# Kernel tuning notes

Hardware: AMD Instinct MI355X
Metric: run time of the kernel (lower is better)

Reference implementation:

```python
import jax, jax.numpy as jnp
import numpy as np

B, IN_DIM, L = 8, 1, 512
D_MODEL, N_LAYERS, D_STATE, HORIZON, D_CONV, EXPAND = 512, 4, 16, 96, 4, 2
D_INNER = EXPAND * D_MODEL            # 1024
DT_RANK = (D_MODEL + 15) // 16        # ceil(d_model/16) = 32
EPS = 1e-5


def setup_inputs() -> dict:
    key = jax.random.key(0)
    ks = jax.random.split(key, 10)
    s = 0.02
    f32 = jnp.float32
    return {
        "x": jax.random.normal(ks[0], (B, IN_DIM, L), f32),
        "embed_w": jax.random.normal(ks[1], (D_MODEL, IN_DIM), f32) * s,
        "embed_b": jnp.zeros((D_MODEL,), f32),
        "norm_w": jnp.ones((N_LAYERS, D_MODEL), f32),
        "in_proj_w": jax.random.normal(ks[2], (N_LAYERS, 2 * D_INNER, D_MODEL), f32) * s,
        "conv_w": jax.random.normal(ks[3], (N_LAYERS, D_INNER, D_CONV), f32) * s,
        "conv_b": jnp.zeros((N_LAYERS, D_INNER), f32),
        "x_proj_w": jax.random.normal(ks[4], (N_LAYERS, DT_RANK + 2 * D_STATE, D_INNER), f32) * s,
        "dt_w": jax.random.normal(ks[5], (N_LAYERS, D_INNER, DT_RANK), f32) * s,
        "dt_b": jax.random.uniform(ks[6], (N_LAYERS, D_INNER), f32, -4.0, -2.0),
        "A_log": jnp.log(jnp.broadcast_to(jnp.arange(1, D_STATE + 1, dtype=f32), (N_LAYERS, D_INNER, D_STATE))),
        "D": jnp.ones((N_LAYERS, D_INNER), f32),
        "out_proj_w": jax.random.normal(ks[7], (N_LAYERS, D_MODEL, D_INNER), f32) * s,
        "head_w": jax.random.normal(ks[8], (HORIZON, D_MODEL), f32) * s,
        "head_b": jnp.zeros((HORIZON,), f32),
    }


def _rmsnorm(x, w):
    return x * jax.lax.rsqrt(jnp.mean(x * x, axis=-1, keepdims=True) + EPS) * w


def _mamba_layer(x, norm_w, in_w, conv_w, conv_b, xproj_w, dt_w, dt_b, A_log, Dp, out_w):
    res = x
    h = _rmsnorm(x, norm_w)
    xz = h @ in_w.T                       # (B, L, 2*I)
    xin, z = jnp.split(xz, 2, axis=-1)
    # causal depthwise conv1d over L (left-pad d_conv-1)
    lhs = jnp.swapaxes(xin, 1, 2)         # (B, I, L)
    rhs = conv_w[:, None, :]              # (I, 1, K)
    conv = jax.lax.conv_general_dilated(
        lhs, rhs, (1,), [(D_CONV - 1, 0)],
        dimension_numbers=("NCH", "OIH", "NCH"), feature_group_count=D_INNER)
    xin = jax.nn.silu(jnp.swapaxes(conv, 1, 2) + conv_b)   # (B, L, I)
    dbc = xin @ xproj_w.T                                   # (B, L, dt_rank+2N)
    delta = jax.nn.softplus(dbc[..., :DT_RANK] @ dt_w.T + dt_b)  # (B, L, I)
    Bc = dbc[..., DT_RANK:DT_RANK + D_STATE]                # (B, L, N)
    Cc = dbc[..., DT_RANK + D_STATE:]                       # (B, L, N)
    A = -jnp.exp(A_log)                                     # (I, N)
    dA = jnp.exp(delta[..., None] * A)                      # (B, L, I, N)
    dBx = delta[..., None] * Bc[:, :, None, :] * xin[..., None]

    def step(hst, inputs):
        a, bx = inputs
        hst = a * hst + bx
        return hst, hst

    h0 = jnp.zeros((x.shape[0], D_INNER, D_STATE), x.dtype)
    _, hs = jax.lax.scan(step, h0, (jnp.swapaxes(dA, 0, 1), jnp.swapaxes(dBx, 0, 1)))
    hs = jnp.swapaxes(hs, 0, 1)                             # (B, L, I, N)
    y = jnp.einsum("blin,bln->bli", hs, Cc) + Dp * xin
    y = y * jax.nn.silu(z)
    return res + y @ out_w.T


def reference(x, embed_w, embed_b, norm_w, in_proj_w, conv_w, conv_b, x_proj_w,
              dt_w, dt_b, A_log, D, out_proj_w, head_w, head_b):
    h = jnp.swapaxes(x, 1, 2) @ embed_w.T + embed_b         # (B, L, d_model)
    for i in range(N_LAYERS):
        h = _mamba_layer(h, norm_w[i], in_proj_w[i], conv_w[i], conv_b[i],
                         x_proj_w[i], dt_w[i], dt_b[i], A_log[i], D[i], out_proj_w[i])
    return h[:, -1, :] @ head_w.T + head_b                  # (B, horizon)
```

## Files before the change

### kernel.cpp

```cpp
#include <hip/hip_runtime.h>
#include <hip/hip_bf16.h>

#define B_  8
#define L_  512
#define DM  512
#define NL  4
#define DS  16
#define HOR 96
#define DC  4
#define DI  1024
#define DTR 32

#define CHUNK 16
#define NCHK (L_/CHUNK)

typedef __bf16 bf16_t;
typedef __bf16 b8_t __attribute__((ext_vector_type(8)));
typedef float  f4_t __attribute__((ext_vector_type(4)));

#define LOG2E 1.44269504088896f

__device__ __forceinline__ float sigmoidf_(float x){ return 1.f/(1.f+__expf(-x)); }

__device__ __forceinline__ void async16(const bf16_t* g, bf16_t* l){
  __builtin_amdgcn_global_load_lds((const __attribute__((address_space(1))) void*)g,
                                   (__attribute__((address_space(3))) void*)l, 16, 0, 0);
}

__global__ __launch_bounds__(256) void k_cvtall(const float* __restrict__ p0, bf16_t* __restrict__ o0,
                                                const float* __restrict__ p1, bf16_t* __restrict__ o1,
                                                const float* __restrict__ p2, bf16_t* __restrict__ o2,
                                                const float* __restrict__ p3, bf16_t* __restrict__ o3){
  int j = blockIdx.x*256 + threadIdx.x;
  const int S0=1048576, S1=65536, S2=32768;
  const float* src; bf16_t* dst;
  if (j < S0){ src=p0; dst=o0; }
  else if ((j-=S0) < S1){ src=p1; dst=o1; }
  else if ((j-=S1) < S2){ src=p2; dst=o2; }
  else { j-=S2; src=p3; dst=o3; }
  f4_t v = ((const f4_t*)src)[j];
  bf16_t* o = dst + (size_t)j*4;
  o[0]=(bf16_t)v[0]; o[1]=(bf16_t)v[1]; o[2]=(bf16_t)v[2]; o[3]=(bf16_t)v[3];
}

__global__ __launch_bounds__(256) void k_embed(const float* __restrict__ x, const float* __restrict__ ew,
                                               const float* __restrict__ eb, float* __restrict__ h){
  int idx = blockIdx.x*256 + threadIdx.x;
  int d = idx & (DM-1); int t = idx >> 9;
  h[idx] = x[t]*ew[d] + eb[d];
}

__global__ __launch_bounds__(256) void k_rms(const float* __restrict__ h, const float* __restrict__ w,
                                             bf16_t* __restrict__ o){
  int t = blockIdx.x; int tid = threadIdx.x;
  const float* hp = h + (size_t)t*DM;
  float v0 = hp[tid], v1 = hp[tid+256];
  float s = v0*v0 + v1*v1;
  #pragma unroll
  for (int m=32;m;m>>=1) s += __shfl_xor(s, m);
  __shared__ float red[4];
  if ((tid&63)==0) red[tid>>6]=s;
  __syncthreads();
  float tot = red[0]+red[1]+red[2]+red[3];
  float sc = rsqrtf(tot*(1.f/DM) + 1e-5f);
  o[(size_t)t*DM + tid]       = (bf16_t)(v0*sc*w[tid]);
  o[(size_t)t*DM + tid + 256] = (bf16_t)(v1*sc*w[tid+256]);
}

__global__ __launch_bounds__(256) void k_g128(const bf16_t* __restrict__ A, int lda,
                                              const bf16_t* __restrict__ W, int ldw,
                                              int K, bf16_t* __restrict__ Cbf, int ldc){
  __shared__ bf16_t As[4*128*32];
  __shared__ bf16_t Ws[4*128*32];
  int tid = threadIdx.x;
  int m0 = blockIdx.y*128, n0 = blockIdx.x*128;
  int wave = tid>>6, lane = tid&63;
  int wm = (wave>>1)*64, wn = (wave&1)*64;
  int lr = lane&15, q = lane>>4;
  int rs = tid>>2, cs = (tid&3)*8;
  f4_t acc[4][4] = {};
  for (int k0=0;k0<K;k0+=128){
    #pragma unroll
    for (int p=0;p<4;p++){
      #pragma unroll
      for (int s=0;s<2;s++){
        int row = s*64 + rs;
        async16(A + (size_t)(m0+row)*lda + k0 + p*32 + cs, As + p*4096 + s*2048 + tid*8);
        async16(W + (size_t)(n0+row)*ldw + k0 + p*32 + cs, Ws + p*4096 + s*2048 + tid*8);
      }
    }
    __syncthreads();
    #pragma unroll
    for (int p=0;p<4;p++){
      b8_t a[4], b[4];
      #pragma unroll
      for (int i=0;i<4;i++) a[i] = *(const b8_t*)(As + p*4096 + (wm+i*16+lr)*32 + q*8);
      #pragma unroll
      for (int j=0;j<4;j++) b[j] = *(const b8_t*)(Ws + p*4096 + (wn+j*16+lr)*32 + q*8);
      #pragma unroll
      for (int i=0;i<4;i++)
        #pragma unroll
        for (int j=0;j<4;j++)
          acc[i][j] = __builtin_amdgcn_mfma_f32_16x16x32_bf16(a[i], b[j], acc[i][j], 0,0,0);
    }
    __syncthreads();
  }
  #pragma unroll
  for (int i=0;i<4;i++)
  #pragma unroll
  for (int j=0;j<4;j++){
    int col = n0 + wn + j*16 + lr;
    int rb  = m0 + wm + i*16 + q*4;
    #pragma unroll
    for (int r=0;r<4;r++)
      Cbf[(size_t)(rb+r)*ldc + col] = (bf16_t)acc[i][j][r];
  }
}

__global__ __launch_bounds__(256) void k_gout64(const bf16_t* __restrict__ A,
                                                const bf16_t* __restrict__ W,
                                                float* __restrict__ C){
  __shared__ bf16_t As[4*64*32];
  __shared__ bf16_t Ws[4*64*32];
  int tid = threadIdx.x;
  int m0 = blockIdx.y*64, n0 = blockIdx.x*64;
  int wave = tid>>6, lane = tid&63;
  int wm = (wave>>1)*32, wn = (wave&1)*32;
  int lr = lane&15, q = lane>>4;
  int e0 = tid*8, r0 = e0>>5, c0 = e0&31;
  f4_t acc[2][2] = {};
  for (int k0=0;k0<DI;k0+=128){
    #pragma unroll
    for (int p=0;p<4;p++){
      async16(A + (size_t)(m0+r0)*DI + k0 + p*32 + c0, As + p*2048 + e0);
      async16(W + (size_t)(n0+r0)*DI + k0 + p*32 + c0, Ws + p*2048 + e0);
    }
    __syncthreads();
    #pragma unroll
    for (int p=0;p<4;p++){
      b8_t a[2], b[2];
      #pragma unroll
      for (int i=0;i<2;i++) a[i] = *(const b8_t*)(As + p*2048 + (wm+i*16+lr)*32 + q*8);
      #pragma unroll
      for (int j=0;j<2;j++) b[j] = *(const b8_t*)(Ws + p*2048 + (wn+j*16+lr)*32 + q*8);
      #pragma unroll
      for (int i=0;i<2;i++)
        #pragma unroll
        for (int j=0;j<2;j++)
          acc[i][j] = __builtin_amdgcn_mfma_f32_16x16x32_bf16(a[i], b[j], acc[i][j], 0,0,0);
    }
    __syncthreads();
  }
  #pragma unroll
  for (int i=0;i<2;i++)
  #pragma unroll
  for (int j=0;j<2;j++){
    int col = n0 + wn + j*16 + lr;
    int rb  = m0 + wm + i*16 + q*4;
    #pragma unroll
    for (int r=0;r<4;r++){
      size_t off = (size_t)(rb+r)*DM + col;
      C[off] = C[off] + acc[i][j][r];
    }
  }
}

__global__ __launch_bounds__(256) void k_dbc(const bf16_t* __restrict__ xzbf, const float* __restrict__ cw,
                                             const float* __restrict__ cb, const bf16_t* __restrict__ wxp,
                                             float* __restrict__ part, bf16_t* __restrict__ xinbf){
  __shared__ bf16_t As[4*64*32];
  __shared__ bf16_t Ws[4*64*32];
  int tid = threadIdx.x;
  int m0 = blockIdx.x*64;
  int z = blockIdx.y;
  int kbase = z*256;
  int wave = tid>>6, lane = tid&63;
  int wm = (wave>>1)*32, wn = (wave&1)*32;
  int lr = lane&15, q = lane>>4;
  int e0 = tid*8, r0 = e0>>5, c0 = e0&31;
  int gt = m0 + r0;
  int l  = gt & (L_-1);
  f4_t acc[2][2] = {};
  for (int k0=0;k0<256;k0+=128){
    #pragma unroll
    for (int p=0;p<4;p++){
      int ch = kbase + k0 + p*32 + c0;
      float cv[8];
      #pragma unroll
      for (int c=0;c<8;c++) cv[c] = cb[ch+c];
      #pragma unroll
      for (int k=0;k<DC;k++){
        if (l + k - (DC-1) >= 0){
          b8_t xv = *(const b8_t*)(xzbf + (size_t)(gt + k - (DC-1))*(2*DI) + ch);
          #pragma unroll
          for (int c=0;c<8;c++) cv[c] += (float)xv[c] * cw[(ch+c)*DC + k];
        }
      }
      b8_t av;
      #pragma unroll
      for (int c=0;c<8;c++){ float s = cv[c]*sigmoidf_(cv[c]); av[c] = (bf16_t)s; }
      *(b8_t*)(As + p*2048 + e0) = av;
      *(b8_t*)(xinbf + (size_t)gt*DI + ch) = av;
      async16(wxp + (size_t)r0*DI + kbase + k0 + p*32 + c0, Ws + p*2048 + e0);
    }
    __syncthreads();
    #pragma unroll
    for (int p=0;p<4;p++){
      b8_t a[2], b[2];
      #pragma unroll
      for (int i=0;i<2;i++) a[i] = *(const b8_t*)(As + p*2048 + (wm+i*16+lr)*32 + q*8);
      #pragma unroll
      for (int j=0;j<2;j++) b[j] = *(const b8_t*)(Ws + p*2048 + (wn+j*16+lr)*32 + q*8);
      #pragma unroll
      for (int i=0;i<2;i++)
        #pragma unroll
        for (int j=0;j<2;j++)
          acc[i][j] = __builtin_amdgcn_mfma_f32_16x16x32_bf16(a[i], b[j], acc[i][j], 0,0,0);
    }
    __syncthreads();
  }
  float* P = part + (size_t)z*(B_*L_*64);
  #pragma unroll
  for (int i=0;i<2;i++)
  #pragma unroll
  for (int j=0;j<2;j++){
    int col = wn + j*16 + lr;
    int rb  = m0 + wm + i*16 + q*4;
    #pragma unroll
    for (int r=0;r<4;r++) P[(size_t)(rb+r)*64 + col] = acc[i][j][r];
  }
}

__global__ __launch_bounds__(256) void k_dt(const float* __restrict__ part, const bf16_t* __restrict__ wdt,
                                            const float* __restrict__ dtb, float* __restrict__ dbc,
                                            bf16_t* __restrict__ delta){
  __shared__ bf16_t As[64*32];
  __shared__ bf16_t Ws[64*32];
  int tid = threadIdx.x;
  int m0 = blockIdx.y*64, n0 = blockIdx.x*64;
  const size_t S = (size_t)B_*L_*64;
  int r0 = tid>>2, c0 = (tid&3)*8;
  int gt = m0 + r0;
  size_t base = (size_t)gt*64 + c0;
  f4_t s0 = *(const f4_t*)(part + base);
  f4_t s1 = *(const f4_t*)(part + base + 4);
  #pragma unroll
  for (int z=1;z<4;z++){
    s0 += *(const f4_t*)(part + z*S + base);
    s1 += *(const f4_t*)(part + z*S + base + 4);
  }
  b8_t av;
  #pragma unroll
  for (int c=0;c<4;c++){ av[c] = (bf16_t)s0[c]; av[4+c] = (bf16_t)s1[c]; }
  *(b8_t*)(As + tid*8) = av;
  if (n0 == 0){
    f4_t t0 = *(const f4_t*)(part + base + 32);
    f4_t t1 = *(const f4_t*)(part + base + 36);
    #pragma unroll
    for (int z=1;z<4;z++){
      t0 += *(const f4_t*)(part + z*S + base + 32);
      t1 += *(const f4_t*)(part + z*S + base + 36);
    }
    *(f4_t*)(dbc + base + 32) = t0;
    *(f4_t*)(dbc + base + 36) = t1;
  }
  async16(wdt + (size_t)(n0+r0)*DTR + c0, Ws + tid*8);
  __syncthreads();
  int wave = tid>>6, lane = tid&63;
  int wm = (wave>>1)*32, wn = (wave&1)*32;
  int lr = lane&15, q = lane>>4;
  b8_t a[2], b[2];
  #pragma unroll
  for (int i=0;i<2;i++) a[i] = *(const b8_t*)(As + (wm+i*16+lr)*32 + q*8);
  #pragma unroll
  for (int j=0;j<2;j++) b[j] = *(const b8_t*)(Ws + (wn+j*16+lr)*32 + q*8);
  f4_t acc[2][2] = {};
  #pragma unroll
  for (int i=0;i<2;i++)
    #pragma unroll
    for (int j=0;j<2;j++)
      acc[i][j] = __builtin_amdgcn_mfma_f32_16x16x32_bf16(a[i], b[j], acc[i][j], 0,0,0);
  #pragma unroll
  for (int i=0;i<2;i++)
  #pragma unroll
  for (int j=0;j<2;j++){
    int col = n0 + wn + j*16 + lr;
    int rb  = m0 + wm + i*16 + q*4;
    #pragma unroll
    for (int r=0;r<4;r++){
      float xv = acc[i][j][r] + dtb[col];
      float v = (xv>20.f)?xv:log1pf(__expf(xv));
      delta[(size_t)(rb+r)*DI + col] = (bf16_t)v;
    }
  }
}

__global__ __launch_bounds__(256) void k_scan_p1(const bf16_t* __restrict__ delta, const bf16_t* __restrict__ xin,
                                                 const float* __restrict__ dbc, const float* __restrict__ Alog,
                                                 bf16_t* __restrict__ hend, bf16_t* __restrict__ aprod){
  __shared__ bf16_t des[CHUNK][256];
  __shared__ bf16_t xs[CHUNK][256];
  __shared__ float Bs[CHUNK][DS];
  int tid = threadIdx.x;
  int blk = blockIdx.x;
  int chgrp = blk & 3;
  int chunk = (blk>>2) & (NCHK-1);
  int b = blk >> 7;
  int ch0 = chgrp<<8;
  int ch = ch0 + tid;
  int t0 = (b<<9) + chunk*CHUNK;
  #pragma unroll
  for (int idx=tid; idx<CHUNK*32; idx+=256){
    int row = idx>>5, c = (idx&31)*8;
    *(b8_t*)(&des[row][c]) = *(const b8_t*)(delta + (size_t)(t0+row)*DI + ch0 + c);
    *(b8_t*)(&xs[row][c])  = *(const b8_t*)(xin   + (size_t)(t0+row)*DI + ch0 + c);
  }
  {
    int ll = tid>>4, n = tid&15;
    Bs[ll][n] = dbc[(t0+ll)*64 + DTR + n];
  }
  __syncthreads();
  float An2[DS], h[DS];
  const f4_t* Ap = (const f4_t*)(Alog + ch*DS);
  #pragma unroll
  for (int v=0;v<4;v++){
    f4_t a4 = Ap[v];
    #pragma unroll
    for (int k=0;k<4;k++){ An2[v*4+k] = -__expf(a4[k])*LOG2E; h[v*4+k]=0.f; }
  }
  float sde = 0.f;
  #pragma unroll
  for (int l=0;l<CHUNK;l++){
    float de = (float)des[l][tid];
    float xv = (float)xs[l][tid];
    float dx = de*xv;
    sde += de;
    #pragma unroll
    for (int n=0;n<DS;n++){
      float dA = exp2f(de*An2[n]);
      h[n] = dA*h[n] + dx*Bs[l][n];
    }
  }
  size_t base = ((size_t)chunk*(B_*DI) + (b<<10) + ch)*DS;
  b8_t hv[2], av[2];
  #pragma unroll
  for (int v=0;v<2;v++)
    #pragma unroll
    for (int k=0;k<8;k++){
      hv[v][k] = (bf16_t)h[v*8+k];
      av[v][k] = (bf16_t)exp2f(An2[v*8+k]*sde);
    }
  ((b8_t*)(hend + base))[0] = hv[0]; ((b8_t*)(hend + base))[1] = hv[1];
  ((b8_t*)(aprod + base))[0] = av[0]; ((b8_t*)(aprod + base))[1] = av[1];
}

__global__ __launch_bounds__(256) void k_scan_p2(const bf16_t* __restrict__ hend, bf16_t* __restrict__ ap_hin){
  int g = blockIdx.x*256 + threadIdx.x;
  float h = 0.f;
  for (int c=0;c<NCHK;c++){
    size_t off = (size_t)c*(B_*DI*DS) + g;
    float a = (float)ap_hin[off];
    float e = (float)hend[off];
    ap_hin[off] = (bf16_t)h;
    h = a*h + e;
  }
}

__global__ __launch_bounds__(256) void k_scan_p3(const bf16_t* __restrict__ delta, const bf16_t* __restrict__ xz,
                                                 const bf16_t* __restrict__ xin,
                                                 const float* __restrict__ dbc, const float* __restrict__ Alog,
                                                 const bf16_t* __restrict__ hin, const float* __restrict__ Dp,
                                                 bf16_t* __restrict__ ybf){
  __shared__ bf16_t des[CHUNK][256];
  __shared__ bf16_t xs[CHUNK][256];
  __shared__ bf16_t zs[CHUNK][256];
  __shared__ float Bs[CHUNK][DS];
  __shared__ float Cs[CHUNK][DS];
  int tid = threadIdx.x;
  int blk = blockIdx.x;
  int chgrp = blk & 3;
  int chunk = (blk>>2) & (NCHK-1);
  int b = blk >> 7;
  int ch0 = chgrp<<8;
  int ch = ch0 + tid;
  int t0 = (b<<9) + chunk*CHUNK;
  #pragma unroll
  for (int idx=tid; idx<CHUNK*32; idx+=256){
    int row = idx>>5, c = (idx&31)*8;
    *(b8_t*)(&des[row][c]) = *(const b8_t*)(delta + (size_t)(t0+row)*DI + ch0 + c);
    *(b8_t*)(&xs[row][c])  = *(const b8_t*)(xin   + (size_t)(t0+row)*DI + ch0 + c);
    *(b8_t*)(&zs[row][c])  = *(const b8_t*)(xz + (size_t)(t0+row)*(2*DI) + DI + ch0 + c);
  }
  {
    int ll = tid>>4, n = tid&15;
    Bs[ll][n] = dbc[(t0+ll)*64 + DTR + n];
    Cs[ll][n] = dbc[(t0+ll)*64 + DTR + DS + n];
  }
  __syncthreads();
  float An2[DS], h[DS];
  const f4_t* Ap = (const f4_t*)(Alog + ch*DS);
  size_t base = ((size_t)chunk*(B_*DI) + (b<<10) + ch)*DS;
  b8_t h0 = ((const b8_t*)(hin + base))[0];
  b8_t h1 = ((const b8_t*)(hin + base))[1];
  #pragma unroll
  for (int v=0;v<4;v++){
    f4_t a4 = Ap[v];
    #pragma unroll
    for (int k=0;k<4;k++){
      An2[v*4+k] = -__expf(a4[k])*LOG2E;
      int idx = v*4+k;
      h[idx] = (idx<8) ? (float)h0[idx] : (float)h1[idx-8];
    }
  }
  float Dv = Dp[ch];
  bf16_t* yp = ybf + (size_t)t0*DI + ch;
  #pragma unroll
  for (int l=0;l<CHUNK;l++){
    float de = (float)des[l][tid];
    float zv = (float)zs[l][tid];
    float xv = (float)xs[l][tid];
    float dx = de*xv;
    float y = 0.f;
    #pragma unroll
    for (int n=0;n<DS;n++){
      float dA = exp2f(de*An2[n]);
      h[n] = dA*h[n] + dx*Bs[l][n];
      y += h[n]*Cs[l][n];
    }
    y = (y + Dv*xv) * (zv * sigmoidf_(zv));
    yp[(size_t)l*DI] = (bf16_t)y;
  }
}

__global__ __launch_bounds__(256) void k_head(const float* __restrict__ h, const float* __restrict__ hw,
                                              const float* __restrict__ hb, float* __restrict__ out){
  int wave = threadIdx.x>>6, lane = threadIdx.x&63;
  int gw = blockIdx.x*4 + wave;
  int b = gw / HOR, hh = gw % HOR;
  const float* hp = h + ((size_t)b*L_ + (L_-1))*DM;
  const float* wp = hw + (size_t)hh*DM;
  float s = 0.f;
  #pragma unroll
  for (int k=0;k<DM;k+=64) s += hp[k+lane]*wp[k+lane];
  #pragma unroll
  for (int m=32;m;m>>=1) s += __shfl_xor(s, m);
  if (lane==0) out[gw] = s + hb[hh];
}

extern "C" void kernel_launch(void* const* d_in, const int* in_sizes, int n_in,
                              void* d_out, int out_size, void* d_ws, size_t ws_size,
                              hipStream_t stream){
  const float* x    = (const float*)d_in[0];
  const float* ew   = (const float*)d_in[1];
  const float* eb   = (const float*)d_in[2];
  const float* nw   = (const float*)d_in[3];
  const float* ipw  = (const float*)d_in[4];
  const float* cw   = (const float*)d_in[5];
  const float* cb   = (const float*)d_in[6];
  const float* xpw  = (const float*)d_in[7];
  const float* dtw  = (const float*)d_in[8];
  const float* dtb  = (const float*)d_in[9];
  const float* alog = (const float*)d_in[10];
  const float* Dp   = (const float*)d_in[11];
  const float* opw  = (const float*)d_in[12];
  const float* hw   = (const float*)d_in[13];
  const float* hb   = (const float*)d_in[14];
  float* out = (float*)d_out;

  char* ws = (char*)d_ws;
  size_t o = 0;
  float*  h      = (float*)(ws + o);  o += (size_t)8<<20;
  bf16_t* hnorm  = (bf16_t*)(ws + o); o += (size_t)4<<20;
  bf16_t* xzbf   = (bf16_t*)(ws + o); o += (size_t)16<<20;
  bf16_t* xinbf  = (bf16_t*)(ws + o); o += (size_t)8<<20;
  bf16_t* delta  = (bf16_t*)(ws + o); o += (size_t)8<<20;
  bf16_t* ybf    = (bf16_t*)(ws + o); o += (size_t)8<<20;
  float*  dbc    = (float*)(ws + o);  o += (size_t)1<<20;
  float*  dbcp   = (float*)(ws + o);  o += (size_t)4<<20;
  bf16_t* w_in   = (bf16_t*)(ws + o); o += (size_t)8<<20;
  bf16_t* w_out  = (bf16_t*)(ws + o); o += (size_t)4<<20;
  bf16_t* w_xp   = (bf16_t*)(ws + o); o += (size_t)1<<19;
  bf16_t* w_dt   = (bf16_t*)(ws + o); o += (size_t)1<<18;
  bf16_t* hend   = (bf16_t*)(ws + o); o += (size_t)8<<20;
  bf16_t* aphin  = (bf16_t*)(ws + o); o += (size_t)8<<20;

  k_cvtall<<<6528,256,0,stream>>>(ipw, w_in, xpw, w_xp, dtw, w_dt, opw, w_out);
  k_embed<<<(B_*L_*DM)/256,256,0,stream>>>(x, ew, eb, h);

  for (int i=0;i<NL;i++){
    k_rms<<<B_*L_,256,0,stream>>>(h, nw + i*DM, hnorm);
    k_g128<<<dim3(2*DI/128, B_*L_/128),256,0,stream>>>(
        hnorm, DM, w_in + (size_t)i*2*DI*DM, DM, DM, xzbf, 2*DI);
    k_dbc<<<dim3(B_*L_/64, 4),256,0,stream>>>(xzbf, cw + i*DI*DC, cb + i*DI,
                                              w_xp + (size_t)i*64*DI, dbcp, xinbf);
    k_dt<<<dim3(DI/64, B_*L_/64),256,0,stream>>>(dbcp, w_dt + (size_t)i*DI*DTR,
                                                 dtb + i*DI, dbc, delta);
    k_scan_p1<<<B_*NCHK*4,256,0,stream>>>(delta, xinbf, dbc, alog + i*DI*DS, hend, aphin);
    k_scan_p2<<<(B_*DI*DS)/256,256,0,stream>>>(hend, aphin);
    k_scan_p3<<<B_*NCHK*4,256,0,stream>>>(delta, xzbf, xinbf, dbc, alog + i*DI*DS,
                                          aphin, Dp + i*DI, ybf);
    k_gout64<<<dim3(DM/64, B_*L_/64),256,0,stream>>>(ybf, w_out + (size_t)i*DM*DI, h);
  }
  k_head<<<(B_*HOR)/4,256,0,stream>>>(h, hw, hb, out);
}
```

Measured before the change: 606.4 us.

## Fuse prep kernels, widen out-proj K step, split dbc over 8 K-slices

Merges weight conversion and embedding into a single launch, with the embedding now written in float4 vectors. The out-projection GEMM now stages 256-wide K tiles, halving its sync count at the cost of doubled LDS per block and likely lower occupancy. The conv+x_proj kernel now splits K into 8 slices of 128 instead of 4 of 256, doubling its block count for more parallelism. In exchange, the dt kernel must sum 8 partial buffers and the partial workspace doubles.

```diff
diff --git a/kernel.cpp b/kernel.cpp
--- a/kernel.cpp
+++ b/kernel.cpp
@@ -27,27 +27,36 @@
                                    (__attribute__((address_space(3))) void*)l, 16, 0, 0);
 }
 
-__global__ __launch_bounds__(256) void k_cvtall(const float* __restrict__ p0, bf16_t* __restrict__ o0,
-                                                const float* __restrict__ p1, bf16_t* __restrict__ o1,
-                                                const float* __restrict__ p2, bf16_t* __restrict__ o2,
-                                                const float* __restrict__ p3, bf16_t* __restrict__ o3){
-  int j = blockIdx.x*256 + threadIdx.x;
-  const int S0=1048576, S1=65536, S2=32768;
-  const float* src; bf16_t* dst;
-  if (j < S0){ src=p0; dst=o0; }
-  else if ((j-=S0) < S1){ src=p1; dst=o1; }
-  else if ((j-=S1) < S2){ src=p2; dst=o2; }
-  else { j-=S2; src=p3; dst=o3; }
-  f4_t v = ((const f4_t*)src)[j];
-  bf16_t* o = dst + (size_t)j*4;
-  o[0]=(bf16_t)v[0]; o[1]=(bf16_t)v[1]; o[2]=(bf16_t)v[2]; o[3]=(bf16_t)v[3];
-}
-
-__global__ __launch_bounds__(256) void k_embed(const float* __restrict__ x, const float* __restrict__ ew,
-                                               const float* __restrict__ eb, float* __restrict__ h){
-  int idx = blockIdx.x*256 + threadIdx.x;
-  int d = idx & (DM-1); int t = idx >> 9;
-  h[idx] = x[t]*ew[d] + eb[d];
+__global__ __launch_bounds__(256) void k_prep(const float* __restrict__ p0, bf16_t* __restrict__ o0,
+                                              const float* __restrict__ p1, bf16_t* __restrict__ o1,
+                                              const float* __restrict__ p2, bf16_t* __restrict__ o2,
+                                              const float* __restrict__ p3, bf16_t* __restrict__ o3,
+                                              const float* __restrict__ x, const float* __restrict__ ew,
+                                              const float* __restrict__ eb, float* __restrict__ h){
+  int blk = blockIdx.x;
+  if (blk < 6528){
+    int j = blk*256 + threadIdx.x;
+    const int S0=1048576, S1=65536, S2=32768;
+    const float* src; bf16_t* dst;
+    if (j < S0){ src=p0; dst=o0; }
+    else if ((j-=S0) < S1){ src=p1; dst=o1; }
+    else if ((j-=S1) < S2){ src=p2; dst=o2; }
+    else { j-=S2; src=p3; dst=o3; }
+    f4_t v = ((const f4_t*)src)[j];
+    bf16_t* o = dst + (size_t)j*4;
+    o[0]=(bf16_t)v[0]; o[1]=(bf16_t)v[1]; o[2]=(bf16_t)v[2]; o[3]=(bf16_t)v[3];
+  } else {
+    int j = (blk-6528)*256 + threadIdx.x;
+    int idx = j*4;
+    int d = idx & (DM-1); int t = idx >> 9;
+    float xv = x[t];
+    f4_t w = *(const f4_t*)(ew + d);
+    f4_t b = *(const f4_t*)(eb + d);
+    f4_t v;
+    #pragma unroll
+    for (int c=0;c<4;c++) v[c] = xv*w[c] + b[c];
+    *(f4_t*)(h + idx) = v;
+  }
 }
 
 __global__ __launch_bounds__(256) void k_rms(const float* __restrict__ h, const float* __restrict__ w,
@@ -120,8 +129,8 @@
 __global__ __launch_bounds__(256) void k_gout64(const bf16_t* __restrict__ A,
                                                 const bf16_t* __restrict__ W,
                                                 float* __restrict__ C){
-  __shared__ bf16_t As[4*64*32];
-  __shared__ bf16_t Ws[4*64*32];
+  __shared__ bf16_t As[8*64*32];
+  __shared__ bf16_t Ws[8*64*32];
   int tid = threadIdx.x;
   int m0 = blockIdx.y*64, n0 = blockIdx.x*64;
   int wave = tid>>6, lane = tid&63;
@@ -129,15 +138,15 @@
   int lr = lane&15, q = lane>>4;
   int e0 = tid*8, r0 = e0>>5, c0 = e0&31;
   f4_t acc[2][2] = {};
-  for (int k0=0;k0<DI;k0+=128){
-    #pragma unroll
-    for (int p=0;p<4;p++){
+  for (int k0=0;k0<DI;k0+=256){
+    #pragma unroll
+    for (int p=0;p<8;p++){
       async16(A + (size_t)(m0+r0)*DI + k0 + p*32 + c0, As + p*2048 + e0);
       async16(W + (size_t)(n0+r0)*DI + k0 + p*32 + c0, Ws + p*2048 + e0);
     }
     __syncthreads();
     #pragma unroll
-    for (int p=0;p<4;p++){
+    for (int p=0;p<8;p++){
       b8_t a[2], b[2];
       #pragma unroll
       for (int i=0;i<2;i++) a[i] = *(const b8_t*)(As + p*2048 + (wm+i*16+lr)*32 + q*8);
@@ -173,7 +182,7 @@
   int tid = threadIdx.x;
   int m0 = blockIdx.x*64;
   int z = blockIdx.y;
-  int kbase = z*256;
+  int kbase = z*128;
   int wave = tid>>6, lane = tid&63;
   int wm = (wave>>1)*32, wn = (wave&1)*32;
   int lr = lane&15, q = lane>>4;
@@ -181,43 +190,40 @@
   int gt = m0 + r0;
   int l  = gt & (L_-1);
   f4_t acc[2][2] = {};
-  for (int k0=0;k0<256;k0+=128){
-    #pragma unroll
-    for (int p=0;p<4;p++){
-      int ch = kbase + k0 + p*32 + c0;
-      float cv[8];
-      #pragma unroll
-      for (int c=0;c<8;c++) cv[c] = cb[ch+c];
-      #pragma unroll
-      for (int k=0;k<DC;k++){
-        if (l + k - (DC-1) >= 0){
-          b8_t xv = *(const b8_t*)(xzbf + (size_t)(gt + k - (DC-1))*(2*DI) + ch);
-          #pragma unroll
-          for (int c=0;c<8;c++) cv[c] += (float)xv[c] * cw[(ch+c)*DC + k];
-        }
+  #pragma unroll
+  for (int p=0;p<4;p++){
+    int ch = kbase + p*32 + c0;
+    float cv[8];
+    #pragma unroll
+    for (int c=0;c<8;c++) cv[c] = cb[ch+c];
+    #pragma unroll
+    for (int k=0;k<DC;k++){
+      if (l + k - (DC-1) >= 0){
+        b8_t xv = *(const b8_t*)(xzbf + (size_t)(gt + k - (DC-1))*(2*DI) + ch);
+        #pragma unroll
+        for (int c=0;c<8;c++) cv[c] += (float)xv[c] * cw[(ch+c)*DC + k];
       }
-      b8_t av;
-      #pragma unroll
-      for (int c=0;c<8;c++){ float s = cv[c]*sigmoidf_(cv[c]); av[c] = (bf16_t)s; }
-      *(b8_t*)(As + p*2048 + e0) = av;
-      *(b8_t*)(xinbf + (size_t)gt*DI + ch) = av;
-      async16(wxp + (size_t)r0*DI + kbase + k0 + p*32 + c0, Ws + p*2048 + e0);
-    }
-    __syncthreads();
-    #pragma unroll
-    for (int p=0;p<4;p++){
-      b8_t a[2], b[2];
-      #pragma unroll
-      for (int i=0;i<2;i++) a[i] = *(const b8_t*)(As + p*2048 + (wm+i*16+lr)*32 + q*8);
-      #pragma unroll
-      for (int j=0;j<2;j++) b[j] = *(const b8_t*)(Ws + p*2048 + (wn+j*16+lr)*32 + q*8);
-      #pragma unroll
-      for (int i=0;i<2;i++)
-        #pragma unroll
-        for (int j=0;j<2;j++)
-          acc[i][j] = __builtin_amdgcn_mfma_f32_16x16x32_bf16(a[i], b[j], acc[i][j], 0,0,0);
-    }
-    __syncthreads();
+    }
+    b8_t av;
+    #pragma unroll
+    for (int c=0;c<8;c++){ float s = cv[c]*sigmoidf_(cv[c]); av[c] = (bf16_t)s; }
+    *(b8_t*)(As + p*2048 + e0) = av;
+    *(b8_t*)(xinbf + (size_t)gt*DI + ch) = av;
+    async16(wxp + (size_t)r0*DI + kbase + p*32 + c0, Ws + p*2048 + e0);
+  }
+  __syncthreads();
+  #pragma unroll
+  for (int p=0;p<4;p++){
+    b8_t a[2], b[2];
+    #pragma unroll
+    for (int i=0;i<2;i++) a[i] = *(const b8_t*)(As + p*2048 + (wm+i*16+lr)*32 + q*8);
+    #pragma unroll
+    for (int j=0;j<2;j++) b[j] = *(const b8_t*)(Ws + p*2048 + (wn+j*16+lr)*32 + q*8);
+    #pragma unroll
+    for (int i=0;i<2;i++)
+      #pragma unroll
+      for (int j=0;j<2;j++)
+        acc[i][j] = __builtin_amdgcn_mfma_f32_16x16x32_bf16(a[i], b[j], acc[i][j], 0,0,0);
   }
   float* P = part + (size_t)z*(B_*L_*64);
   #pragma unroll
@@ -245,7 +251,7 @@
   f4_t s0 = *(const f4_t*)(part + base);
   f4_t s1 = *(const f4_t*)(part + base + 4);
   #pragma unroll
-  for (int z=1;z<4;z++){
+  for (int z=1;z<8;z++){
     s0 += *(const f4_t*)(part + z*S + base);
     s1 += *(const f4_t*)(part + z*S + base + 4);
   }
@@ -257,7 +263,7 @@
     f4_t t0 = *(const f4_t*)(part + base + 32);
     f4_t t1 = *(const f4_t*)(part + base + 36);
     #pragma unroll
-    for (int z=1;z<4;z++){
+    for (int z=1;z<8;z++){
       t0 += *(const f4_t*)(part + z*S + base + 32);
       t1 += *(const f4_t*)(part + z*S + base + 36);
     }
@@ -476,7 +482,7 @@
   bf16_t* delta  = (bf16_t*)(ws + o); o += (size_t)8<<20;
   bf16_t* ybf    = (bf16_t*)(ws + o); o += (size_t)8<<20;
   float*  dbc    = (float*)(ws + o);  o += (size_t)1<<20;
-  float*  dbcp   = (float*)(ws + o);  o += (size_t)4<<20;
+  float*  dbcp   = (float*)(ws + o);  o += (size_t)8<<20;
   bf16_t* w_in   = (bf16_t*)(ws + o); o += (size_t)8<<20;
   bf16_t* w_out  = (bf16_t*)(ws + o); o += (size_t)4<<20;
   bf16_t* w_xp   = (bf16_t*)(ws + o); o += (size_t)1<<19;
@@ -484,14 +490,14 @@
   bf16_t* hend   = (bf16_t*)(ws + o); o += (size_t)8<<20;
   bf16_t* aphin  = (bf16_t*)(ws + o); o += (size_t)8<<20;
 
-  k_cvtall<<<6528,256,0,stream>>>(ipw, w_in, xpw, w_xp, dtw, w_dt, opw, w_out);
-  k_embed<<<(B_*L_*DM)/256,256,0,stream>>>(x, ew, eb, h);
+  k_prep<<<8576,256,0,stream>>>(ipw, w_in, xpw, w_xp, dtw, w_dt, opw, w_out,
+                                x, ew, eb, h);
 
   for (int i=0;i<NL;i++){
     k_rms<<<B_*L_,256,0,stream>>>(h, nw + i*DM, hnorm);
     k_g128<<<dim3(2*DI/128, B_*L_/128),256,0,stream>>>(
         hnorm, DM, w_in + (size_t)i*2*DI*DM, DM, DM, xzbf, 2*DI);
-    k_dbc<<<dim3(B_*L_/64, 4),256,0,stream>>>(xzbf, cw + i*DI*DC, cb + i*DI,
+    k_dbc<<<dim3(B_*L_/64, 8),256,0,stream>>>(xzbf, cw + i*DI*DC, cb + i*DI,
                                               w_xp + (size_t)i*64*DI, dbcp, xinbf);
     k_dt<<<dim3(DI/64, B_*L_/64),256,0,stream>>>(dbcp, w_dt + (size_t)i*DI*DTR,
                                                  dtb + i*DI, dbc, delta);
```

Result: no change. 606.7 us, median of 2 (+0.0%).
